# Kernel optimization log

Hardware: AMD Instinct MI355X
Metric: run time of the kernel (lower is better)

## Reference

```python
import jax, jax.numpy as jnp
import numpy as np


def rotate_half(x):
    d = x.shape[-1] // 2
    return jnp.concatenate([-x[..., d:], x[..., :d]], axis=-1)


def setup_inputs() -> dict:
    key = jax.random.key(0)
    ks = jax.random.split(key, 8)
    B, T, C, H = 2, 2048, 2048, 16
    hd = C // H
    x = jax.random.normal(ks[0], (B, T, C), dtype=jnp.float32)
    # realistic RoPE tables
    inv_freq = 1.0 / (10000.0 ** (jnp.arange(0, hd, 2, dtype=jnp.float32) / hd))
    t = jnp.arange(T, dtype=jnp.float32)
    freqs = jnp.einsum('t,f->tf', t, inv_freq)
    emb = jnp.concatenate([freqs, freqs], axis=-1)  # [T, hd]
    cos = jnp.cos(emb)
    sin = jnp.sin(emb)
    mask = jnp.tril(jnp.ones((T, T), dtype=bool))[None, None]  # causal [1,1,T,T]
    s = C ** -0.5
    Wq = jax.random.normal(ks[1], (C, C), dtype=jnp.float32) * s
    Wk = jax.random.normal(ks[2], (C, C), dtype=jnp.float32) * s
    Wv = jax.random.normal(ks[3], (C, C), dtype=jnp.float32) * s
    Wo = jax.random.normal(ks[4], (C, C), dtype=jnp.float32) * s
    return {"x": x, "cos": cos, "sin": sin, "mask": mask,
            "Wq": Wq, "Wk": Wk, "Wv": Wv, "Wo": Wo}


def reference(x, cos, sin, mask, Wq, Wk, Wv, Wo):
    B, T, C = x.shape
    H = 16
    hd = C // H
    scale = hd ** -0.5
    # projections: torch Linear stores W as [out,in], y = x @ W^T
    def proj(W):
        return jnp.einsum('btc,dc->btd', x, W).reshape(B, T, H, hd).transpose(0, 2, 1, 3)
    q, k, v = proj(Wq), proj(Wk), proj(Wv)  # [B,H,T,hd]
    c = cos[None, None]  # [1,1,T,hd]
    s = sin[None, None]
    q = q * c + rotate_half(q) * s
    k = k * c + rotate_half(k) * s
    attn = jnp.einsum('bhqd,bhkd->bhqk', q, k) * scale
    attn = jnp.where(mask, attn, -jnp.inf)
    attn = jax.nn.softmax(attn, axis=-1)
    out = jnp.einsum('bhqk,bhkd->bhqd', attn, v)
    out = out.transpose(0, 2, 1, 3).reshape(B, T, C)
    return jnp.einsum('btc,dc->btd', out, Wo)
```

## Files before the change

kernel.cpp:

```cpp
#include <hip/hip_runtime.h>
#include <cstdint>

typedef __bf16 bf16_t;
typedef __bf16 bf16x8 __attribute__((ext_vector_type(8)));
typedef __bf16 bf16x4 __attribute__((ext_vector_type(4)));
typedef float  f32x4  __attribute__((ext_vector_type(4)));

#define BB 2
#define TT 2048
#define CC 2048
#define HH 16
#define HD 128

static __device__ __forceinline__ void async_copy16(const void* gp, void* lp) {
  __builtin_amdgcn_global_load_lds(
      (const __attribute__((address_space(1))) void*)(uintptr_t)gp,
      (__attribute__((address_space(3))) void*)(uint32_t)(uintptr_t)lp,
      16, 0, 0);
}

__global__ __launch_bounds__(256)
void cast_all(const float* __restrict__ x, const float* __restrict__ wq,
              const float* __restrict__ wk, const float* __restrict__ wv,
              const float* __restrict__ wo, bf16_t* __restrict__ xb,
              bf16_t* __restrict__ wq_b) {
  const int NX4 = (BB * TT * CC) / 4;
  const int NW4 = (CC * CC) / 4;
  int i = blockIdx.x * 256 + threadIdx.x;
  const float* s;
  bf16_t* d;
  int off;
  if (i < NX4) {
    s = x; d = xb; off = i;
  } else {
    int j = i - NX4;
    int w = j >> 20;
    off = j & (NW4 - 1);
    s = (w == 0) ? wq : (w == 1) ? wk : (w == 2) ? wv : wo;
    d = wq_b + (size_t)w * (CC * CC);
  }
  float4 v = ((const float4*)s)[off];
  bf16x4 o;
  o[0] = (bf16_t)v.x; o[1] = (bf16_t)v.y; o[2] = (bf16_t)v.z; o[3] = (bf16_t)v.w;
  ((bf16x4*)d)[off] = o;
}

template <int MODE>
__global__ __launch_bounds__(256)
void gemm_bt(const bf16_t* __restrict__ A, const bf16_t* __restrict__ Bw,
             void* __restrict__ C0, void* __restrict__ C1, void* __restrict__ C2,
             int Kdim, int Ndim) {
  __shared__ __align__(16) char smem[128 * 136 * 2];
  bf16_t* As = (bf16_t*)smem;
  bf16_t* Bs = (bf16_t*)(smem + 16384);
  const int tid  = threadIdx.x;
  const int wave = tid >> 6, lane = tid & 63;
  const int quad = lane >> 4, l16 = lane & 15;
  const int m0 = blockIdx.y * 128, n0 = blockIdx.x * 128;
  const int wm = (wave >> 1) * 64, wn = (wave & 1) * 64;

  f32x4 acc[4][4] = {};

  const int srow = lane >> 3;
  const int scol = (((lane & 7) ^ srow) & 7) * 8;
  const int swz  = (l16 & 7) * 8;

  for (int k0 = 0; k0 < Kdim; k0 += 64) {
#pragma unroll
    for (int i = 0; i < 4; ++i) {
      int chunk = wave * 4 + i;
      int row = chunk * 8 + srow;
      async_copy16(A + (size_t)(m0 + row) * Kdim + k0 + scol, As + chunk * 512);
    }
#pragma unroll
    for (int i = 0; i < 4; ++i) {
      int chunk = wave * 4 + i;
      int row = chunk * 8 + srow;
      async_copy16(Bw + (size_t)(n0 + row) * Kdim + k0 + scol, Bs + chunk * 512);
    }
    __syncthreads();
#pragma unroll
    for (int kk = 0; kk < 64; kk += 32) {
      const int koff = (kk + quad * 8) ^ swz;
      bf16x8 af[4], bfr[4];
#pragma unroll
      for (int i = 0; i < 4; ++i)
        af[i] = *(const bf16x8*)&As[(wm + i * 16 + l16) * 64 + koff];
#pragma unroll
      for (int j = 0; j < 4; ++j)
        bfr[j] = *(const bf16x8*)&Bs[(wn + j * 16 + l16) * 64 + koff];
#pragma unroll
      for (int i = 0; i < 4; ++i)
#pragma unroll
        for (int j = 0; j < 4; ++j)
          acc[i][j] = __builtin_amdgcn_mfma_f32_16x16x32_bf16(af[i], bfr[j], acc[i][j], 0, 0, 0);
    }
    __syncthreads();
  }

  if (MODE == 0) {
#pragma unroll
    for (int i = 0; i < 4; ++i)
#pragma unroll
      for (int j = 0; j < 4; ++j) {
        int gcol = n0 + wn + j * 16 + l16;
#pragma unroll
        for (int r = 0; r < 4; ++r) {
          int grow = m0 + wm + i * 16 + quad * 4 + r;
          ((float*)C0)[(size_t)grow * Ndim + gcol] = acc[i][j][r];
        }
      }
  } else {
    const int h = (n0 & (CC - 1)) >> 7;
    bf16_t* Ct = (bf16_t*)smem;
    __syncthreads();
#pragma unroll
    for (int i = 0; i < 4; ++i)
#pragma unroll
      for (int j = 0; j < 4; ++j) {
        int c = wn + j * 16 + l16;
#pragma unroll
        for (int r = 0; r < 4; ++r)
          Ct[(wm + i * 16 + quad * 4 + r) * 136 + c] = (bf16_t)acc[i][j][r];
      }
    __syncthreads();
    const unsigned short* Cu = (const unsigned short*)Ct;
    int col = tid >> 1;
    int rh  = (tid & 1) * 64;
    int grow0 = m0 + rh;
    int b = grow0 >> 11, t0 = grow0 & (TT - 1);
    unsigned int pk[32];
#pragma unroll
    for (int s = 0; s < 32; ++s) {
      unsigned int lo = Cu[(rh + 2 * s) * 136 + col];
      unsigned int hi = Cu[(rh + 2 * s + 1) * 136 + col];
      pk[s] = lo | (hi << 16);
    }
    bf16_t* dstp = (bf16_t*)C2 + ((size_t)(b * HH + h) * HD + col) * TT + t0;
#pragma unroll
    for (int u = 0; u < 8; ++u) {
      uint4 w; w.x = pk[4*u]; w.y = pk[4*u+1]; w.z = pk[4*u+2]; w.w = pk[4*u+3];
      *(uint4*)(dstp + 8 * u) = w;
    }
  }
}

__global__ __launch_bounds__(512, 2)
void gemm_qkv256(const bf16_t* __restrict__ A, const bf16_t* __restrict__ Bw,
                 bf16_t* __restrict__ Qo, bf16_t* __restrict__ Ko, int Kdim) {
  extern __shared__ __align__(16) char smem[];
  bf16_t* lds = (bf16_t*)smem;
  const int tid  = threadIdx.x;
  const int wave = tid >> 6, lane = tid & 63;
  const int quad = lane >> 4, l16 = lane & 15;
  const int wm = wave >> 2, wn = wave & 3;
  const int n0 = blockIdx.x * 256, m0 = blockIdx.y * 256;

  const int srow = lane >> 3;
  const int scol = ((lane & 7) ^ srow) * 8;
  const int swz  = (l16 & 7) * 8;
  const int nK = Kdim >> 6;

  const bf16_t* Ag = A  + (size_t)(m0 + wave * 32 + srow) * Kdim + scol;
  const bf16_t* Bg = Bw + (size_t)(n0 + wave * 32 + srow) * Kdim + scol;
  const int ldsChunk = wave * 4 * 512;

#define STAGE_A(kt, buf)                                                      \
  {                                                                           \
    bf16_t* dstA = lds + (buf) * 32768 + ldsChunk;                            \
    const bf16_t* srcA = Ag + (kt) * 64;                                      \
    _Pragma("unroll")                                                         \
    for (int ci = 0; ci < 4; ++ci)                                            \
      async_copy16(srcA + (size_t)(ci * 8) * Kdim, dstA + ci * 512);          \
  }
#define STAGE_B(kt, buf)                                                      \
  {                                                                           \
    bf16_t* dstB = lds + (buf) * 32768 + 16384 + ldsChunk;                    \
    const bf16_t* srcB = Bg + (kt) * 64;                                      \
    _Pragma("unroll")                                                         \
    for (int ci = 0; ci < 4; ++ci)                                            \
      async_copy16(srcB + (size_t)(ci * 8) * Kdim, dstB + ci * 512);          \
  }

  f32x4 acc[8][4] = {};

  STAGE_A(0, 0); STAGE_B(0, 0); STAGE_A(1, 1); STAGE_B(1, 1);

  const int k0off = (quad * 8) ^ swz;
  const int k1off = (32 + quad * 8) ^ swz;

  for (int k = 0; k < nK; ++k) {
    const int cur = k & 1;
    const bf16_t* Asb = lds + cur * 32768;
    const bf16_t* Bsb = Asb + 16384;
    if (k < nK - 1) asm volatile("s_waitcnt vmcnt(8)" ::: "memory");
    else            asm volatile("s_waitcnt vmcnt(0)" ::: "memory");
    __builtin_amdgcn_s_barrier();
    __builtin_amdgcn_sched_barrier(0);

    bf16x8 a0[8], b0[4], a1[8], b1[4];
#pragma unroll
    for (int i = 0; i < 8; ++i)
      a0[i] = *(const bf16x8*)&Asb[(wm * 128 + i * 16 + l16) * 64 + k0off];
#pragma unroll
    for (int j = 0; j < 4; ++j)
      b0[j] = *(const bf16x8*)&Bsb[(wn * 64 + j * 16 + l16) * 64 + k0off];
    asm volatile("s_waitcnt lgkmcnt(0)" ::: "memory");
    __builtin_amdgcn_sched_barrier(0);
    __builtin_amdgcn_s_setprio(1);
#pragma unroll
    for (int i = 0; i < 4; ++i)
#pragma unroll
      for (int j = 0; j < 4; ++j)
        acc[i][j] = __builtin_amdgcn_mfma_f32_16x16x32_bf16(a0[i], b0[j], acc[i][j], 0, 0, 0);
    __builtin_amdgcn_s_setprio(0);

#pragma unroll
    for (int i = 0; i < 8; ++i)
      a1[i] = *(const bf16x8*)&Asb[(wm * 128 + i * 16 + l16) * 64 + k1off];
#pragma unroll
    for (int j = 0; j < 4; ++j)
      b1[j] = *(const bf16x8*)&Bsb[(wn * 64 + j * 16 + l16) * 64 + k1off];
    __builtin_amdgcn_s_setprio(1);
#pragma unroll
    for (int i = 4; i < 8; ++i)
#pragma unroll
      for (int j = 0; j < 4; ++j)
        acc[i][j] = __builtin_amdgcn_mfma_f32_16x16x32_bf16(a0[i], b0[j], acc[i][j], 0, 0, 0);
    __builtin_amdgcn_s_setprio(0);
    asm volatile("s_waitcnt lgkmcnt(0)" ::: "memory");
    __builtin_amdgcn_s_barrier();
    __builtin_amdgcn_sched_barrier(0);

    if (k + 2 < nK) STAGE_A(k + 2, cur);
    __builtin_amdgcn_s_setprio(1);
#pragma unroll
    for (int i = 0; i < 4; ++i)
#pragma unroll
      for (int j = 0; j < 4; ++j)
        acc[i][j] = __builtin_amdgcn_mfma_f32_16x16x32_bf16(a1[i], b1[j], acc[i][j], 0, 0, 0);
    __builtin_amdgcn_s_setprio(0);

    if (k + 2 < nK) STAGE_B(k + 2, cur);
    __builtin_amdgcn_s_setprio(1);
#pragma unroll
    for (int i = 4; i < 8; ++i)
#pragma unroll
      for (int j = 0; j < 4; ++j)
        acc[i][j] = __builtin_amdgcn_mfma_f32_16x16x32_bf16(a1[i], b1[j], acc[i][j], 0, 0, 0);
    __builtin_amdgcn_s_setprio(0);
  }
#undef STAGE_A
#undef STAGE_B

  const int proj = n0 >> 11;
  bf16_t* dst = proj == 0 ? Qo : Ko;
#pragma unroll
  for (int i = 0; i < 8; ++i)
#pragma unroll
    for (int j = 0; j < 4; ++j) {
      int colv = (n0 & (CC - 1)) + wn * 64 + j * 16 + l16;
      int h = colv >> 7, d = colv & (HD - 1);
#pragma unroll
      for (int r = 0; r < 4; ++r) {
        int grow = m0 + wm * 128 + i * 16 + quad * 4 + r;
        int b = grow >> 11, t = grow & (TT - 1);
        dst[(((size_t)(b * HH + h) * TT + t) * HD) + d] = (bf16_t)acc[i][j][r];
      }
    }
}

__global__ __launch_bounds__(256) void rope_kernel(bf16_t* __restrict__ Q, bf16_t* __restrict__ K,
                                                   const float* __restrict__ cosT,
                                                   const float* __restrict__ sinT) {
  int idx = blockIdx.x * 256 + threadIdx.x;
  int g  = idx & 7;
  int t  = (idx >> 3) & (TT - 1);
  int bh = idx >> 14;
  int d0 = g * 8;
  size_t base = ((size_t)bh * TT + t) * HD;

  float4 cl0 = *(const float4*)(cosT + t * HD + d0);
  float4 cl1 = *(const float4*)(cosT + t * HD + d0 + 4);
  float4 sl0 = *(const float4*)(sinT + t * HD + d0);
  float4 sl1 = *(const float4*)(sinT + t * HD + d0 + 4);
  float4 ch0 = *(const float4*)(cosT + t * HD + 64 + d0);
  float4 ch1 = *(const float4*)(cosT + t * HD + 64 + d0 + 4);
  float4 sh0 = *(const float4*)(sinT + t * HD + 64 + d0);
  float4 sh1 = *(const float4*)(sinT + t * HD + 64 + d0 + 4);
  float cl[8] = {cl0.x, cl0.y, cl0.z, cl0.w, cl1.x, cl1.y, cl1.z, cl1.w};
  float sl[8] = {sl0.x, sl0.y, sl0.z, sl0.w, sl1.x, sl1.y, sl1.z, sl1.w};
  float ch[8] = {ch0.x, ch0.y, ch0.z, ch0.w, ch1.x, ch1.y, ch1.z, ch1.w};
  float sh[8] = {sh0.x, sh0.y, sh0.z, sh0.w, sh1.x, sh1.y, sh1.z, sh1.w};

  bf16x8 qlo = *(const bf16x8*)(Q + base + d0);
  bf16x8 qhi = *(const bf16x8*)(Q + base + 64 + d0);
  bf16x8 klo = *(const bf16x8*)(K + base + d0);
  bf16x8 khi = *(const bf16x8*)(K + base + 64 + d0);
  bf16x8 qlo2, qhi2, klo2, khi2;
#pragma unroll
  for (int e = 0; e < 8; ++e) {
    float ql = (float)qlo[e], qh = (float)qhi[e];
    qlo2[e] = (bf16_t)(ql * cl[e] - qh * sl[e]);
    qhi2[e] = (bf16_t)(qh * ch[e] + ql * sh[e]);
    float kl = (float)klo[e], kh = (float)khi[e];
    klo2[e] = (bf16_t)(kl * cl[e] - kh * sl[e]);
    khi2[e] = (bf16_t)(kh * ch[e] + kl * sh[e]);
  }
  *(bf16x8*)(Q + base + d0)      = qlo2;
  *(bf16x8*)(Q + base + 64 + d0) = qhi2;
  *(bf16x8*)(K + base + d0)      = klo2;
  *(bf16x8*)(K + base + 64 + d0) = khi2;
}

__global__ __launch_bounds__(512, 2)
void attn_kernel(const bf16_t* __restrict__ Q, const bf16_t* __restrict__ K,
                 const bf16_t* __restrict__ Vt, bf16_t* __restrict__ Out) {
  __shared__ __align__(16) bf16_t Ks[2][64 * 128];
  __shared__ __align__(16) bf16_t Vs[2][128 * 64];
  __shared__ __align__(16) bf16_t Pl[8][16 * 72];
  const int lane = threadIdx.x & 63, wave = threadIdx.x >> 6;
  const int quad = lane >> 4, l16 = lane & 15;
  const int linear = blockIdx.x;
  const int hb = linear & 31;
  const int h = hb & (HH - 1), b = hb >> 4;
  const int spair = linear >> 5;
  const size_t qkbase = (size_t)(b * HH + h) * TT * HD;
  const bf16_t* Kh = K + qkbase;
  const bf16_t* Vh = Vt + (size_t)(b * HH + h) * HD * TT;
  const float scale = 0.08838834764831845f;

  const int srK = lane >> 4;
  const int sgK = lane & 15;
  const int scK0 = (sgK ^ srK) * 8;
  const int scK1 = (sgK ^ (4 + srK)) * 8;
  const int srV = lane >> 3;
  const int scV = (((lane & 7) ^ srV) & 7) * 8;
  const int swz = (l16 & 7) * 8;

#pragma unroll
  for (int half = 0; half < 2; ++half) {
    const int qt = half == 0 ? (15 - spair) : spair;
    const int q0 = qt * 128 + wave * 16;
    const int nIter = qt * 2 + 2;

    bf16x8 qf[4];
    {
      const bf16_t* qrow = Q + qkbase + (size_t)(q0 + l16) * HD;
#pragma unroll
      for (int kc = 0; kc < 4; ++kc) qf[kc] = *(const bf16x8*)(qrow + kc * 32 + quad * 8);
    }

    f32x4 o[8] = {};
    float l_i[4] = {};

    {
#pragma unroll
      for (int i = 0; i < 2; ++i) {
        int chunk = wave * 2 + i;
        int sc = (chunk & 1) ? scK1 : scK0;
        async_copy16(Kh + (size_t)(chunk * 4 + srK) * HD + sc, &Ks[0][chunk * 512]);
      }
#pragma unroll
      for (int i = 0; i < 2; ++i) {
        int chunk = wave * 2 + i;
        async_copy16(Vh + (size_t)(chunk * 8 + srV) * TT + scV, &Vs[0][chunk * 512]);
      }
    }

    for (int it = 0; it < nIter; ++it) {
      const int cur = it & 1;
      const int key0 = it * 64;
      __syncthreads();

      if (it + 1 < nIter) {
        const int nxt = cur ^ 1;
        const int knxt = key0 + 64;
#pragma unroll
        for (int i = 0; i < 2; ++i) {
          int chunk = wave * 2 + i;
          int sc = (chunk & 1) ? scK1 : scK0;
          async_copy16(Kh + (size_t)(knxt + chunk * 4 + srK) * HD + sc, &Ks[nxt][chunk * 512]);
        }
#pragma unroll
        for (int i = 0; i < 2; ++i) {
          int chunk = wave * 2 + i;
          async_copy16(Vh + (size_t)(chunk * 8 + srV) * TT + knxt + scV, &Vs[nxt][chunk * 512]);
        }
      }

      f32x4 s[4] = {};
#pragma unroll
      for (int kc = 0; kc < 4; ++kc) {
        const int koff = (kc * 32 + quad * 8) ^ swz;
#pragma unroll
        for (int kt = 0; kt < 4; ++kt) {
          bf16x8 kf = *(const bf16x8*)&Ks[cur][(kt * 16 + l16) * 128 + koff];
          s[kt] = __builtin_amdgcn_mfma_f32_16x16x32_bf16(qf[kc], kf, s[kt], 0, 0, 0);
        }
      }

      {
        bf16_t* pl = &Pl[wave][0];
#pragma unroll
        for (int r = 0; r < 4; ++r) {
          int rel = q0 + quad * 4 + r - key0;
          int prow = (quad * 4 + r) * 72;
          float lr = 0.f;
#pragma unroll
          for (int kt = 0; kt < 4; ++kt) {
            int c16 = kt * 16 + l16;
            float e = (c16 > rel) ? 0.f : __expf(s[kt][r] * scale);
            lr += e;
            pl[prow + c16] = (bf16_t)e;
          }
          l_i[r] += lr;
        }
      }

      bf16x8 pf0 = *(const bf16x8*)&Pl[wave][l16 * 72 + quad * 8];
      bf16x8 pf1 = *(const bf16x8*)&Pl[wave][l16 * 72 + 32 + quad * 8];
      const int voff0 = (quad * 8) ^ swz;
      const int voff1 = (32 + quad * 8) ^ swz;
#pragma unroll
      for (int n = 0; n < 8; ++n) {
        bf16x8 vf0 = *(const bf16x8*)&Vs[cur][(n * 16 + l16) * 64 + voff0];
        bf16x8 vf1 = *(const bf16x8*)&Vs[cur][(n * 16 + l16) * 64 + voff1];
        o[n] = __builtin_amdgcn_mfma_f32_16x16x32_bf16(pf0, vf0, o[n], 0, 0, 0);
        o[n] = __builtin_amdgcn_mfma_f32_16x16x32_bf16(pf1, vf1, o[n], 0, 0, 0);
      }
    }

#pragma unroll
    for (int r = 0; r < 4; ++r) {
      float l = l_i[r];
#pragma unroll
      for (int off = 1; off < 16; off <<= 1) l += __shfl_xor(l, off);
      l_i[r] = 1.f / l;
    }

#pragma unroll
    for (int n = 0; n < 8; ++n)
#pragma unroll
      for (int r = 0; r < 4; ++r) {
        int qg = q0 + quad * 4 + r;
        size_t off = ((size_t)(b * TT + qg) * CC) + h * HD + n * 16 + l16;
        Out[off] = (bf16_t)(o[n][r] * l_i[r]);
      }
  }
}

extern "C" void kernel_launch(void* const* d_in, const int* in_sizes, int n_in,
                              void* d_out, int out_size, void* d_ws, size_t ws_size,
                              hipStream_t stream) {
  const float* x    = (const float*)d_in[0];
  const float* cosT = (const float*)d_in[1];
  const float* sinT = (const float*)d_in[2];
  const float* Wq = (const float*)d_in[4];
  const float* Wk = (const float*)d_in[5];
  const float* Wv = (const float*)d_in[6];
  const float* Wo = (const float*)d_in[7];
  float* out = (float*)d_out;

  char* ws = (char*)d_ws;
  const size_t XSZ = (size_t)BB * TT * CC * 2;
  const size_t WSZ = (size_t)CC * CC * 2;
  bf16_t* x_bf  = (bf16_t*)(ws);
  bf16_t* wq_bf = (bf16_t*)(ws + XSZ);
  bf16_t* wv_bf = (bf16_t*)(ws + XSZ + 2 * WSZ);
  bf16_t* wo_bf = (bf16_t*)(ws + XSZ + 3 * WSZ);
  bf16_t* Qb    = (bf16_t*)(ws + XSZ + 4 * WSZ);
  bf16_t* Kb    = (bf16_t*)(ws + 2 * XSZ + 4 * WSZ);
  bf16_t* Vt    = (bf16_t*)(ws + 3 * XSZ + 4 * WSZ);
  bf16_t* attn_bf = x_bf;

  const int NX = BB * TT * CC;
  const int NW = CC * CC;
  cast_all<<<(NX / 4 + 4 * (NW / 4)) / 256, 256, 0, stream>>>(
      x, Wq, Wk, Wv, Wo, x_bf, wq_bf);

  (void)hipFuncSetAttribute(reinterpret_cast<const void*>(gemm_qkv256),
                            hipFuncAttributeMaxDynamicSharedMemorySize, 131072);
  gemm_qkv256<<<dim3(2 * CC / 256, BB * TT / 256), 512, 131072, stream>>>(
      x_bf, wq_bf, Qb, Kb, CC);

  gemm_bt<1><<<dim3(CC / 128, BB * TT / 128), 256, 0, stream>>>(
      x_bf, wv_bf, nullptr, nullptr, Vt, CC, CC);

  rope_kernel<<<(BB * HH * TT * 8) / 256, 256, 0, stream>>>(Qb, Kb, cosT, sinT);

  attn_kernel<<<dim3(BB * HH * 8), 512, 0, stream>>>(Qb, Kb, Vt, attn_bf);

  gemm_bt<0><<<dim3(CC / 128, BB * TT / 128), 256, 0, stream>>>(
      attn_bf, wo_bf, out, nullptr, nullptr, CC, CC);
}
```

Before: 370.7 us.

## Fuse RoPE into QKV GEMM epilogue via LDS-staged coalesced stores

The QKV GEMM epilogue now writes its accumulator tile into LDS with padded rows. Each thread then takes one head-row of 128 elements, applies the rotary cos/sin rotation, and writes 16-byte vectors straight to the Q/K layout. This removes the separate RoPE kernel's full read-modify-write pass over Q and K, and replaces scattered 2-byte epilogue stores with coalesced vector stores. Separately, the attention P staging buffer row stride is padded from 72 to 76 to change the LDS bank mapping. Both new paddings give row strides that are not 16-byte aligned, so the 128-bit LDS reads may be split or run slower. Dynamic LDS for the GEMM also grows slightly.

```diff
diff --git a/kernel.cpp b/kernel.cpp
--- a/kernel.cpp
+++ b/kernel.cpp
@@ -147,7 +147,9 @@
 
 __global__ __launch_bounds__(512, 2)
 void gemm_qkv256(const bf16_t* __restrict__ A, const bf16_t* __restrict__ Bw,
-                 bf16_t* __restrict__ Qo, bf16_t* __restrict__ Ko, int Kdim) {
+                 bf16_t* __restrict__ Qo, bf16_t* __restrict__ Ko,
+                 const float* __restrict__ cosT, const float* __restrict__ sinT,
+                 int Kdim) {
   extern __shared__ __align__(16) char smem[];
   bf16_t* lds = (bf16_t*)smem;
   const int tid  = threadIdx.x;
@@ -253,64 +255,59 @@
 #undef STAGE_A
 #undef STAGE_B
 
-  const int proj = n0 >> 11;
-  bf16_t* dst = proj == 0 ? Qo : Ko;
-#pragma unroll
-  for (int i = 0; i < 8; ++i)
-#pragma unroll
-    for (int j = 0; j < 4; ++j) {
-      int colv = (n0 & (CC - 1)) + wn * 64 + j * 16 + l16;
-      int h = colv >> 7, d = colv & (HD - 1);
-#pragma unroll
-      for (int r = 0; r < 4; ++r) {
-        int grow = m0 + wm * 128 + i * 16 + quad * 4 + r;
-        int b = grow >> 11, t = grow & (TT - 1);
-        dst[(((size_t)(b * HH + h) * TT + t) * HD) + d] = (bf16_t)acc[i][j][r];
-      }
-    }
-}
-
-__global__ __launch_bounds__(256) void rope_kernel(bf16_t* __restrict__ Q, bf16_t* __restrict__ K,
-                                                   const float* __restrict__ cosT,
-                                                   const float* __restrict__ sinT) {
-  int idx = blockIdx.x * 256 + threadIdx.x;
-  int g  = idx & 7;
-  int t  = (idx >> 3) & (TT - 1);
-  int bh = idx >> 14;
-  int d0 = g * 8;
-  size_t base = ((size_t)bh * TT + t) * HD;
-
-  float4 cl0 = *(const float4*)(cosT + t * HD + d0);
-  float4 cl1 = *(const float4*)(cosT + t * HD + d0 + 4);
-  float4 sl0 = *(const float4*)(sinT + t * HD + d0);
-  float4 sl1 = *(const float4*)(sinT + t * HD + d0 + 4);
-  float4 ch0 = *(const float4*)(cosT + t * HD + 64 + d0);
-  float4 ch1 = *(const float4*)(cosT + t * HD + 64 + d0 + 4);
-  float4 sh0 = *(const float4*)(sinT + t * HD + 64 + d0);
-  float4 sh1 = *(const float4*)(sinT + t * HD + 64 + d0 + 4);
-  float cl[8] = {cl0.x, cl0.y, cl0.z, cl0.w, cl1.x, cl1.y, cl1.z, cl1.w};
-  float sl[8] = {sl0.x, sl0.y, sl0.z, sl0.w, sl1.x, sl1.y, sl1.z, sl1.w};
-  float ch[8] = {ch0.x, ch0.y, ch0.z, ch0.w, ch1.x, ch1.y, ch1.z, ch1.w};
-  float sh[8] = {sh0.x, sh0.y, sh0.z, sh0.w, sh1.x, sh1.y, sh1.z, sh1.w};
-
-  bf16x8 qlo = *(const bf16x8*)(Q + base + d0);
-  bf16x8 qhi = *(const bf16x8*)(Q + base + 64 + d0);
-  bf16x8 klo = *(const bf16x8*)(K + base + d0);
-  bf16x8 khi = *(const bf16x8*)(K + base + 64 + d0);
-  bf16x8 qlo2, qhi2, klo2, khi2;
-#pragma unroll
-  for (int e = 0; e < 8; ++e) {
-    float ql = (float)qlo[e], qh = (float)qhi[e];
-    qlo2[e] = (bf16_t)(ql * cl[e] - qh * sl[e]);
-    qhi2[e] = (bf16_t)(qh * ch[e] + ql * sh[e]);
-    float kl = (float)klo[e], kh = (float)khi[e];
-    klo2[e] = (bf16_t)(kl * cl[e] - kh * sl[e]);
-    khi2[e] = (bf16_t)(kh * ch[e] + kl * sh[e]);
-  }
-  *(bf16x8*)(Q + base + d0)      = qlo2;
-  *(bf16x8*)(Q + base + 64 + d0) = qhi2;
-  *(bf16x8*)(K + base + d0)      = klo2;
-  *(bf16x8*)(K + base + 64 + d0) = khi2;
+  {
+    const int proj = n0 >> 11;
+    bf16_t* dst = proj == 0 ? Qo : Ko;
+    bf16_t* Ct = lds;
+#pragma unroll
+    for (int i = 0; i < 8; ++i)
+#pragma unroll
+      for (int j = 0; j < 4; ++j) {
+        int coll = wn * 64 + j * 16 + l16;
+        int pcol = coll + ((coll >> 7) << 2);
+#pragma unroll
+        for (int r = 0; r < 4; ++r) {
+          int rowl = wm * 128 + i * 16 + quad * 4 + r;
+          Ct[rowl * 268 + pcol] = (bf16_t)acc[i][j][r];
+        }
+      }
+    __syncthreads();
+    const int rowl = tid >> 1, hh = tid & 1;
+    const int t = (m0 + rowl) & (TT - 1);
+    const int b = m0 >> 11;
+    const int h = ((n0 & (CC - 1)) >> 7) + hh;
+    const bf16_t* src = Ct + rowl * 268 + hh * 132;
+    bf16_t* drow = dst + (((size_t)(b * HH + h) * TT + t) * HD);
+    const float* ct = cosT + t * HD;
+    const float* st = sinT + t * HD;
+#pragma unroll
+    for (int g = 0; g < 8; ++g) {
+      int d0 = g * 8;
+      bf16x8 lo = *(const bf16x8*)(src + d0);
+      bf16x8 hi = *(const bf16x8*)(src + 64 + d0);
+      float4 cl0 = *(const float4*)(ct + d0);
+      float4 cl1 = *(const float4*)(ct + d0 + 4);
+      float4 sl0 = *(const float4*)(st + d0);
+      float4 sl1 = *(const float4*)(st + d0 + 4);
+      float4 ch0 = *(const float4*)(ct + 64 + d0);
+      float4 ch1 = *(const float4*)(ct + 64 + d0 + 4);
+      float4 sh0 = *(const float4*)(st + 64 + d0);
+      float4 sh1 = *(const float4*)(st + 64 + d0 + 4);
+      float cl[8] = {cl0.x, cl0.y, cl0.z, cl0.w, cl1.x, cl1.y, cl1.z, cl1.w};
+      float sl[8] = {sl0.x, sl0.y, sl0.z, sl0.w, sl1.x, sl1.y, sl1.z, sl1.w};
+      float ch[8] = {ch0.x, ch0.y, ch0.z, ch0.w, ch1.x, ch1.y, ch1.z, ch1.w};
+      float sh[8] = {sh0.x, sh0.y, sh0.z, sh0.w, sh1.x, sh1.y, sh1.z, sh1.w};
+      bf16x8 olo, ohi;
+#pragma unroll
+      for (int e = 0; e < 8; ++e) {
+        float vl = (float)lo[e], vh = (float)hi[e];
+        olo[e] = (bf16_t)(vl * cl[e] - vh * sl[e]);
+        ohi[e] = (bf16_t)(vh * ch[e] + vl * sh[e]);
+      }
+      *(bf16x8*)(drow + d0)      = olo;
+      *(bf16x8*)(drow + 64 + d0) = ohi;
+    }
+  }
 }
 
 __global__ __launch_bounds__(512, 2)
@@ -318,7 +315,7 @@
                  const bf16_t* __restrict__ Vt, bf16_t* __restrict__ Out) {
   __shared__ __align__(16) bf16_t Ks[2][64 * 128];
   __shared__ __align__(16) bf16_t Vs[2][128 * 64];
-  __shared__ __align__(16) bf16_t Pl[8][16 * 72];
+  __shared__ __align__(16) bf16_t Pl[8][16 * 76];
   const int lane = threadIdx.x & 63, wave = threadIdx.x >> 6;
   const int quad = lane >> 4, l16 = lane & 15;
   const int linear = blockIdx.x;
@@ -405,7 +402,7 @@
 #pragma unroll
         for (int r = 0; r < 4; ++r) {
           int rel = q0 + quad * 4 + r - key0;
-          int prow = (quad * 4 + r) * 72;
+          int prow = (quad * 4 + r) * 76;
           float lr = 0.f;
 #pragma unroll
           for (int kt = 0; kt < 4; ++kt) {
@@ -418,8 +415,8 @@
         }
       }
 
-      bf16x8 pf0 = *(const bf16x8*)&Pl[wave][l16 * 72 + quad * 8];
-      bf16x8 pf1 = *(const bf16x8*)&Pl[wave][l16 * 72 + 32 + quad * 8];
+      bf16x8 pf0 = *(const bf16x8*)&Pl[wave][l16 * 76 + quad * 8];
+      bf16x8 pf1 = *(const bf16x8*)&Pl[wave][l16 * 76 + 32 + quad * 8];
       const int voff0 = (quad * 8) ^ swz;
       const int voff1 = (32 + quad * 8) ^ swz;
 #pragma unroll
@@ -480,15 +477,13 @@
       x, Wq, Wk, Wv, Wo, x_bf, wq_bf);
 
   (void)hipFuncSetAttribute(reinterpret_cast<const void*>(gemm_qkv256),
-                            hipFuncAttributeMaxDynamicSharedMemorySize, 131072);
-  gemm_qkv256<<<dim3(2 * CC / 256, BB * TT / 256), 512, 131072, stream>>>(
-      x_bf, wq_bf, Qb, Kb, CC);
+                            hipFuncAttributeMaxDynamicSharedMemorySize, 137216);
+  gemm_qkv256<<<dim3(2 * CC / 256, BB * TT / 256), 512, 137216, stream>>>(
+      x_bf, wq_bf, Qb, Kb, cosT, sinT, CC);
 
   gemm_bt<1><<<dim3(CC / 128, BB * TT / 128), 256, 0, stream>>>(
       x_bf, wv_bf, nullptr, nullptr, Vt, CC, CC);
 
-  rope_kernel<<<(BB * HH * TT * 8) / 256, 256, 0, stream>>>(Qb, Kb, cosT, sinT);
-
   attn_kernel<<<dim3(BB * HH * 8), 512, 0, stream>>>(Qb, Kb, Vt, attn_bf);
 
   gemm_bt<0><<<dim3(CC / 128, BB * TT / 128), 256, 0, stream>>>(
```

Measured after the change: 389.2 us. +5.0%, slower.
